# Kernel tuning notes

Hardware: AMD Instinct MI355X
Metric: run time of the kernel (lower is better)

The kernel has to match this reference:

```python
import math
import jax, jax.numpy as jnp
import numpy as np

# --- Cayley-Dickson octonion structure constants: e_i * e_j = sign * e_{i XOR j} ---
def _cd_tables(levels=3):
    idx = np.array([[0]]); sgn = np.array([[1]])
    for _ in range(levels):
        n = idx.shape[0]; N = 2 * n
        I = np.zeros((N, N), np.int64); S = np.zeros((N, N), np.int64)
        cj = lambda j: 1 if j == 0 else -1  # conj sign of basis element j
        for i in range(n):
            for j in range(n):
                I[i, j] = idx[i, j];             S[i, j] = sgn[i, j]
                I[i, n + j] = n + idx[j, i];     S[i, n + j] = sgn[j, i]
                I[n + i, j] = n + idx[i, j];     S[n + i, j] = sgn[i, j] * cj(j)
                I[n + i, n + j] = idx[j, i];     S[n + i, n + j] = -cj(j) * sgn[j, i]
        idx, sgn = I, S
    return idx, sgn

_OIDX, _OSGN = _cd_tables()
# Octonion-structured linear: out_i = sum_j SIGN[i,j] * x_j @ W[WIDX[i,j]], WIDX[i,j]=i^j
_WIDX = np.array([[i ^ j for j in range(8)] for i in range(8)], np.int64)
_SIGN = np.array([[_OSGN[j, i ^ j] for j in range(8)] for i in range(8)], np.float32)


def _oct_linear(x, W):
    # x: [B,T,C], W: [8, C/8, C/8]
    B, T, C = x.shape
    Cp = C // 8
    parts = x.reshape(B, T, 8, Cp)
    Weff = jnp.asarray(_SIGN)[:, :, None, None] * W[jnp.asarray(_WIDX)]  # [8,8,Cp,Cp]
    return jnp.einsum('btjp,ijpq->btiq', parts, Weff).reshape(B, T, C)


def _rope(x, cos, sin):
    # x: [B,T,H,D]; consecutive channel pairs form complex numbers
    B, T, H, D = x.shape
    xr = x.reshape(B, T, H, D // 2, 2)
    xe, xo = xr[..., 0], xr[..., 1]
    c = cos[None, :, None, :]
    s = sin[None, :, None, :]
    return jnp.stack([xe * c - xo * s, xe * s + xo * c], axis=-1).reshape(B, T, H, D)


def _forward(x, Wq, Wk, Wv, Wo, mixer_W, mixer_beta, freqs_cos, freqs_sin):
    B, T, C = x.shape
    H = 32; D = C // H
    q = _oct_linear(x, Wq).reshape(B, T, H, D)
    k = _oct_linear(x, Wk).reshape(B, T, H, D)
    v = _oct_linear(x, Wv).reshape(B, T, H, D)
    q = _rope(q, freqs_cos, freqs_sin)
    k = _rope(k, freqs_cos, freqs_sin)
    q = q.transpose(0, 2, 1, 3)  # [B,H,T,D]
    k = k.transpose(0, 2, 1, 3)
    v = v.transpose(0, 2, 1, 3)
    scores = jnp.einsum('bhqd,bhkd->bhqk', q, k) / jnp.sqrt(jnp.float32(D))
    mask = jnp.tril(jnp.ones((T, T), bool))
    scores = jnp.where(mask, scores, jnp.finfo(scores.dtype).min)
    y = jnp.einsum('bhqk,bhkd->bhqd', jax.nn.softmax(scores, axis=-1), v)  # [B,H,T,D]
    # octonion head mixing in groups of 8 heads
    G = H // 8
    yg = y.reshape(B, G, 8, T, D)
    Weff = jnp.asarray(_SIGN)[:, :, None, None] * mixer_W[jnp.asarray(_WIDX)]  # [8,8,D,D]
    mixed = jnp.einsum('bgjtd,ijde->bgite', yg, Weff) * mixer_beta
    y = mixed.reshape(B, H, T, D).transpose(0, 2, 1, 3).reshape(B, T, C)
    return _oct_linear(y, Wo)


def setup_inputs() -> dict:
    key = jax.random.key(0)
    ks = jax.random.split(key, 8)
    B, T, C, H = 1, 2048, 4096, 32
    D = C // H; Cp = C // 8
    x = jax.random.normal(ks[0], (B, T, C), jnp.float32)
    Wq = jax.random.normal(ks[1], (8, Cp, Cp), jnp.float32) * 0.02
    Wk = jax.random.normal(ks[2], (8, Cp, Cp), jnp.float32) * 0.02
    Wv = jax.random.normal(ks[3], (8, Cp, Cp), jnp.float32) * 0.02
    Wo = jax.random.normal(ks[4], (8, Cp, Cp), jnp.float32) * 0.02
    mixer_W = jax.random.normal(ks[5], (8, D, D), jnp.float32) * 0.02
    mixer_beta = jnp.ones((D,), jnp.float32) * np.float32(math.sqrt(3.0 / (2.0 * D)))
    half = D // 2
    inv = 1.0 / (10000.0 ** (np.arange(half) * 2.0 / D))
    ang = np.arange(T)[:, None] * inv[None, :]
    freqs_cos = jnp.asarray(np.cos(ang), jnp.float32)
    freqs_sin = jnp.asarray(np.sin(ang), jnp.float32)
    return dict(x=x, Wq=Wq, Wk=Wk, Wv=Wv, Wo=Wo, mixer_W=mixer_W,
                mixer_beta=mixer_beta, freqs_cos=freqs_cos, freqs_sin=freqs_sin)


def reference(x, Wq, Wk, Wv, Wo, mixer_W, mixer_beta, freqs_cos, freqs_sin):
    return _forward(x, Wq, Wk, Wv, Wo, mixer_W, mixer_beta, freqs_cos, freqs_sin)
```

## Files before the change

### kernel.cpp

```cpp
#include <hip/hip_runtime.h>

typedef float f32x4 __attribute__((ext_vector_type(4)));
typedef __bf16 bf16x8 __attribute__((ext_vector_type(8)));
typedef unsigned short u16;
typedef u16 u16x8 __attribute__((ext_vector_type(8)));

__constant__ float c_osgn[64] = {
  1, 1, 1, 1, 1, 1, 1, 1,
  1,-1, 1,-1, 1,-1,-1, 1,
  1,-1,-1, 1, 1, 1,-1,-1,
  1, 1,-1,-1, 1,-1, 1,-1,
  1,-1,-1,-1,-1, 1, 1, 1,
  1, 1,-1, 1,-1,-1,-1, 1,
  1, 1, 1,-1,-1, 1,-1,-1,
  1,-1, 1, 1,-1,-1, 1,-1
};

__device__ __forceinline__ u16 f2bf(float f) {
  union { float f; unsigned u; } v; v.f = f;
  unsigned u = v.u;
  return (u16)((u + 0x7fffu + ((u >> 16) & 1u)) >> 16);
}
__device__ __forceinline__ float bf2f(u16 h) {
  union { unsigned u; float f; } v; v.u = ((unsigned)h) << 16;
  return v.f;
}

typedef const __attribute__((address_space(1))) void* as1cv;
typedef __attribute__((address_space(3))) void* as3v;
__device__ __forceinline__ void load16_lds(const void* g, void* l) {
  __builtin_amdgcn_global_load_lds((as1cv)g, (as3v)l, 16, 0, 0);
}

__global__ void conv_f32_bf16_vec(const float* __restrict__ src, u16* __restrict__ dst) {
  int i = blockIdx.x * 256 + threadIdx.x;
  float4 v = ((const float4*)src)[i];
  ushort4 o; o.x = f2bf(v.x); o.y = f2bf(v.y); o.z = f2bf(v.z); o.w = f2bf(v.w);
  ((ushort4*)dst)[i] = o;
}

__global__ __launch_bounds__(256) void transpose_w2(const float* __restrict__ W,
                                                    u16* __restrict__ Wt) {
  __shared__ float t[64][65];
  const int w = blockIdx.z, p0 = blockIdx.y * 64, q0 = blockIdx.x * 64;
  const float* src = W + ((long)w * 512 + p0) * 512 + q0;
  const int tid = threadIdx.x;
  const int r = tid >> 2, c0 = (tid & 3) * 16;
#pragma unroll
  for (int j = 0; j < 4; j++) {
    float4 v = *(const float4*)(src + (long)r * 512 + c0 + j * 4);
    t[r][c0 + j * 4 + 0] = v.x; t[r][c0 + j * 4 + 1] = v.y;
    t[r][c0 + j * 4 + 2] = v.z; t[r][c0 + j * 4 + 3] = v.w;
  }
  __syncthreads();
  u16* dst = Wt + ((long)w * 512 + q0) * 512 + p0;
#pragma unroll
  for (int j = 0; j < 2; j++) {
    u16x8 o;
#pragma unroll
    for (int k = 0; k < 8; k++) o[k] = f2bf(t[c0 + j * 8 + k][r]);
    *(u16x8*)(dst + (long)r * 512 + c0 + j * 8) = o;
  }
}

__global__ void transpose_wm(const float* __restrict__ W, const float* __restrict__ beta,
                             u16* __restrict__ Wt) {
  int idx = blockIdx.x * 256 + threadIdx.x;
  int w = idx >> 14, rem = idx & 16383;
  int e = rem >> 7, d = rem & 127;
  Wt[(w << 14) + (e << 7) + d] = f2bf(W[(w << 14) + (d << 7) + e] * beta[e]);
}

template <int MODE>
__global__ __launch_bounds__(512, 2) void oct_gemm2f(
    const u16* __restrict__ A, const u16* __restrict__ WtB,
    void* __restrict__ out0, void* __restrict__ out1, void* __restrict__ out2,
    const float* __restrict__ fc, const float* __restrict__ fs,
    int K, int lda, int ldo,
    int slab_shift, int bs_shift, long wslab, long oslab, long acolslab)
{
  __shared__ u16 As[2][256][64];
  __shared__ u16 Bs[2][128][64];
  const int NT = K >> 6;
  const int BS = 1 << bs_shift;
  const long wblk = (long)BS * BS;

  const int nwg = gridDim.x * gridDim.y;
  const int lin = blockIdx.y * gridDim.x + blockIdx.x;
  const int swz = (lin & 7) * (nwg >> 3) + (lin >> 3);
  const int bx = swz % gridDim.x, by = swz / gridDim.x;

  const int nglob = bx * 128;
  const int z = nglob >> slab_shift;
  const int np = nglob & ((1 << slab_shift) - 1);
  const int bi = np >> bs_shift;
  const int nsub = np & (BS - 1);
  const int bm = by * 256;
  const u16* Wt = WtB + (long)z * wslab;
  const long acol0 = (long)z * acolslab;

  const int tid = threadIdx.x;
  const int lane = tid & 63, w = tid >> 6;
  const int l15 = lane & 15, lg = lane >> 4;
  const int wm = w >> 1, wn = w & 1;
  const int srow = lane >> 3;
  const int sgr  = (lane & 7) ^ srow;

  f32x4 acc[4][4];
#pragma unroll
  for (int a = 0; a < 4; a++)
#pragma unroll
    for (int b = 0; b < 4; b++) acc[a][b] = f32x4{0.f, 0.f, 0.f, 0.f};

  auto stage = [&](int t, int buf) {
    const int k0 = t << 6;
    const int widx = bi ^ (k0 >> bs_shift);
    const int kl = k0 & (BS - 1);
    const u16* Wsrc = Wt + (long)widx * wblk + kl;
#pragma unroll
    for (int i = 0; i < 4; i++) {
      const int r = w * 32 + i * 8;
      const u16* g = A + (long)(bm + r + srow) * lda + acol0 + k0 + sgr * 8;
      load16_lds(g, (void*)&As[buf][r][0]);
    }
#pragma unroll
    for (int i = 0; i < 2; i++) {
      const int r = w * 16 + i * 8;
      const u16* g = Wsrc + (long)(nsub + r + srow) * BS + sgr * 8;
      load16_lds(g, (void*)&Bs[buf][r][0]);
    }
  };

  stage(0, 0);
  stage(1, 1);

  for (int t = 0; t < NT; ++t) {
    if (t + 1 < NT) asm volatile("s_waitcnt vmcnt(6)" ::: "memory");
    else            asm volatile("s_waitcnt vmcnt(0)" ::: "memory");
    __builtin_amdgcn_s_barrier();
    asm volatile("" ::: "memory");

    const int cur = t & 1;
    const int bj = t >> (bs_shift - 6);
    const unsigned xm = (c_osgn[bj * 8 + (bi ^ bj)] < 0.f) ? 0x80008000u : 0u;

#pragma unroll
    for (int kk = 0; kk < 64; kk += 32) {
      const int gsw = (((kk >> 3) + lg) ^ (l15 & 7)) * 8;
      uint4 a4[4];
      bf16x8 bF[4];
#pragma unroll
      for (int mt = 0; mt < 4; mt++)
        a4[mt] = *(const uint4*)&As[cur][wm * 64 + mt * 16 + l15][gsw];
      if (xm) {
#pragma unroll
        for (int mt = 0; mt < 4; mt++) {
          a4[mt].x ^= xm; a4[mt].y ^= xm; a4[mt].z ^= xm; a4[mt].w ^= xm;
        }
      }
#pragma unroll
      for (int nt = 0; nt < 4; nt++)
        bF[nt] = *(const bf16x8*)&Bs[cur][wn * 64 + nt * 16 + l15][gsw];
#pragma unroll
      for (int mt = 0; mt < 4; mt++)
#pragma unroll
        for (int nt = 0; nt < 4; nt++)
          acc[mt][nt] = __builtin_amdgcn_mfma_f32_16x16x32_bf16(
              *(const bf16x8*)&a4[mt], bF[nt], acc[mt][nt], 0, 0, 0);
    }

    asm volatile("" ::: "memory");
    __builtin_amdgcn_s_barrier();
    asm volatile("" ::: "memory");
    if (t + 2 < NT) stage(t + 2, cur);
  }

  if constexpr (MODE == 1) {
    if (z == 2) {
      u16* vg = (u16*)out2;
#pragma unroll
      for (int mt = 0; mt < 4; mt++)
#pragma unroll
        for (int nt = 0; nt < 4; nt++)
#pragma unroll
          for (int j = 0; j < 4; j++) {
            const int row = bm + wm * 64 + mt * 16 + 4 * lg + j;
            const int col = np + wn * 64 + nt * 16 + l15;
            vg[(long)row * 4096 + col] = f2bf(acc[mt][nt][j]);
          }
    } else {
      u16* dq = (u16*)(z == 0 ? out0 : out1);
      const int h = np >> 7;
#pragma unroll
      for (int mt = 0; mt < 4; mt++)
#pragma unroll
        for (int nt = 0; nt < 4; nt++) {
          const int d = wn * 64 + nt * 16 + l15;
          const int p = d >> 1;
          const bool ev = (l15 & 1) == 0;
#pragma unroll
          for (int j = 0; j < 4; j++) {
            const int trow = bm + wm * 64 + mt * 16 + 4 * lg + j;
            const float v = acc[mt][nt][j];
            const float sh = __shfl_xor(v, 1);
            const float c = fc[trow * 64 + p];
            const float s = fs[trow * 64 + p];
            const float o = ev ? (v * c - sh * s) : (sh * s + v * c);
            dq[((long)h * 2048 + trow) * 128 + d] = f2bf(o);
          }
        }
    }
  } else {
#pragma unroll
    for (int mt = 0; mt < 4; mt++)
#pragma unroll
      for (int nt = 0; nt < 4; nt++)
#pragma unroll
        for (int j = 0; j < 4; j++) {
          const int row = bm + wm * 64 + mt * 16 + 4 * lg + j;
          const int col = np + wn * 64 + nt * 16 + l15;
          const float v = acc[mt][nt][j];
          if constexpr (MODE == 0)
            ((u16*)out0)[(long)z * oslab + (long)row * ldo + col] = f2bf(v);
          else
            ((float*)out0)[(long)row * ldo + col] = v;
        }
  }
}

__global__ void v_transpose(const u16* __restrict__ vg, u16* __restrict__ vT)
{
  int h = blockIdx.x, t0 = blockIdx.y * 64;
  __shared__ u16 lds[64][136];
  int tid = threadIdx.x;
  int rr = tid >> 4, ch = (tid & 15) * 8;
#pragma unroll
  for (int p = 0; p < 4; p++) {
    int row = p * 16 + rr;
    *(uint4*)&lds[row][ch] = *(const uint4*)(vg + (long)(t0 + row) * 4096 + h * 128 + ch);
  }
  __syncthreads();
  int dd = tid >> 3, tc = (tid & 7) * 8;
#pragma unroll
  for (int p = 0; p < 4; p++) {
    int d = p * 32 + dd;
    u16x8 o;
#pragma unroll
    for (int j = 0; j < 8; j++) o[j] = lds[tc + j][d];
    *(u16x8*)(vT + ((long)h * 128 + d) * 2048 + t0 + tc) = o;
  }
}

__global__ __launch_bounds__(256, 2) void attn3(
    const u16* __restrict__ qR, const u16* __restrict__ kR,
    const u16* __restrict__ vT, u16* __restrict__ y)
{
  const int bid = blockIdx.x;
  const int h = bid & 31;
  const int u = bid >> 5;
  const int qb = (u < 8) ? (u * 2) : (31 - u * 2);
  const int q0 = qb * 128;

  const int tid = threadIdx.x;
  const int lane = tid & 63, w = tid >> 6;
  const int l15 = lane & 15, lg = lane >> 4;

  __shared__ u16 Ks[2][64][128];
  __shared__ u16 Vs[2][128][64];
  __shared__ u16 Ps[4][32][64];

  auto stageK = [&](int kb, int buf) {
    const long kbase = (long)h * 2048 + (long)kb * 64;
#pragma unroll
    for (int i = 0; i < 4; i++) {
      const int j = w * 4 + i;
      const int row = j * 4 + (lane >> 4);
      const int sg = (lane & 15) ^ (row & 7);
      load16_lds(kR + (kbase + row) * 128 + sg * 8, (void*)&Ks[buf][j * 4][0]);
    }
  };
  auto stageV = [&](int kb, int buf) {
    const long vbase = (long)h * 128 * 2048 + (long)kb * 64;
#pragma unroll
    for (int i = 0; i < 4; i++) {
      const int j = w * 4 + i;
      const int row = j * 8 + (lane >> 3);
      const int sg = (lane & 7) ^ (row & 7);
      load16_lds(vT + vbase + (long)row * 2048 + sg * 8, (void*)&Vs[buf][j * 8][0]);
    }
  };

  stageK(0, 0);
  stageV(0, 0);

  bf16x8 aQ[2][4];
#pragma unroll
  for (int rs = 0; rs < 2; rs++) {
    const long qbase = ((long)h * 2048 + q0 + w * 32 + rs * 16 + l15) * 128;
#pragma unroll
    for (int c = 0; c < 4; c++)
      aQ[rs][c] = *(const bf16x8*)(qR + qbase + 32 * c + 8 * lg);
  }

  float m[2][4], lsum[2][4];
  f32x4 Y[2][8];
#pragma unroll
  for (int rs = 0; rs < 2; rs++)
#pragma unroll
    for (int rr = 0; rr < 4; rr++) { m[rs][rr] = -1e30f; lsum[rs][rr] = 0.f; }
#pragma unroll
  for (int rs = 0; rs < 2; rs++)
#pragma unroll
    for (int dt = 0; dt < 8; dt++) Y[rs][dt] = f32x4{0.f, 0.f, 0.f, 0.f};

  const float scale = 0.08838834764831845f;
  const int nkb = 2 * qb + 2;

  for (int kb = 0; kb < nkb; kb++) {
    const int buf = kb & 1;
    const int k0 = kb * 64;
    if (kb + 1 < nkb) { stageK(kb + 1, buf ^ 1); stageV(kb + 1, buf ^ 1); }
    if (kb + 1 < nkb) asm volatile("s_waitcnt vmcnt(8)" ::: "memory");
    else              asm volatile("s_waitcnt vmcnt(0)" ::: "memory");
    __builtin_amdgcn_s_barrier();
    asm volatile("" ::: "memory");

    f32x4 S[2][4];
#pragma unroll
    for (int rs = 0; rs < 2; rs++)
#pragma unroll
      for (int ks = 0; ks < 4; ks++) S[rs][ks] = f32x4{0.f, 0.f, 0.f, 0.f};
#pragma unroll
    for (int c = 0; c < 4; c++) {
      bf16x8 bK[4];
#pragma unroll
      for (int ks = 0; ks < 4; ks++)
        bK[ks] = *(const bf16x8*)&Ks[buf][ks * 16 + l15][(((4 * c + lg) ^ (l15 & 7)) * 8)];
#pragma unroll
      for (int rs = 0; rs < 2; rs++)
#pragma unroll
        for (int ks = 0; ks < 4; ks++)
          S[rs][ks] = __builtin_amdgcn_mfma_f32_16x16x32_bf16(aQ[rs][c], bK[ks], S[rs][ks], 0, 0, 0);
    }

#pragma unroll
    for (int rs = 0; rs < 2; rs++) {
      const int qrow0 = q0 + w * 32 + rs * 16 + 4 * lg;
#pragma unroll
      for (int ks = 0; ks < 4; ks++) {
        const int kg = k0 + ks * 16 + l15;
#pragma unroll
        for (int rr = 0; rr < 4; rr++) {
          float s = S[rs][ks][rr] * scale;
          S[rs][ks][rr] = (kg > qrow0 + rr) ? -1e30f : s;
        }
      }
      float sf[4];
      bool need = false;
#pragma unroll
      for (int rr = 0; rr < 4; rr++) {
        float mx = fmaxf(fmaxf(S[rs][0][rr], S[rs][1][rr]),
                         fmaxf(S[rs][2][rr], S[rs][3][rr]));
#pragma unroll
        for (int off = 1; off < 16; off <<= 1) mx = fmaxf(mx, __shfl_xor(mx, off));
        const bool upd = (mx > m[rs][rr] + 8.f);
        const float mn = upd ? mx : m[rs][rr];
        const float sc = upd ? __expf(m[rs][rr] - mn) : 1.f;
        need |= upd;
        m[rs][rr] = mn;
        float rsum = 0.f;
#pragma unroll
        for (int ks = 0; ks < 4; ks++) {
          float e = __expf(S[rs][ks][rr] - mn);
          S[rs][ks][rr] = e;
          rsum += e;
        }
#pragma unroll
        for (int off = 1; off < 16; off <<= 1) rsum += __shfl_xor(rsum, off);
        lsum[rs][rr] = lsum[rs][rr] * sc + rsum;
        sf[rr] = sc;
      }
      if (__any(need)) {
#pragma unroll
        for (int dt = 0; dt < 8; dt++) {
          f32x4 yv = Y[rs][dt];
          yv[0] *= sf[0]; yv[1] *= sf[1]; yv[2] *= sf[2]; yv[3] *= sf[3];
          Y[rs][dt] = yv;
        }
      }
#pragma unroll
      for (int ks = 0; ks < 4; ks++)
#pragma unroll
        for (int rr = 0; rr < 4; rr++) {
          const int row = rs * 16 + 4 * lg + rr;
          const int G = (2 * ks + (l15 >> 3)) ^ (row & 7);
          Ps[w][row][G * 8 + (l15 & 7)] = f2bf(S[rs][ks][rr]);
        }
    }

#pragma unroll
    for (int kk = 0; kk < 2; kk++) {
      const int pg = ((4 * kk + lg) ^ (l15 & 7)) * 8;
      bf16x8 pF0 = *(const bf16x8*)&Ps[w][l15][pg];
      bf16x8 pF1 = *(const bf16x8*)&Ps[w][16 + l15][pg];
#pragma unroll
      for (int dt = 0; dt < 8; dt++) {
        bf16x8 vF = *(const bf16x8*)&Vs[buf][dt * 16 + l15][pg];
        Y[0][dt] = __builtin_amdgcn_mfma_f32_16x16x32_bf16(pF0, vF, Y[0][dt], 0, 0, 0);
        Y[1][dt] = __builtin_amdgcn_mfma_f32_16x16x32_bf16(pF1, vF, Y[1][dt], 0, 0, 0);
      }
    }
    asm volatile("" ::: "memory");
    __builtin_amdgcn_s_barrier();
    asm volatile("" ::: "memory");
  }

#pragma unroll
  for (int rs = 0; rs < 2; rs++) {
    float inv[4];
#pragma unroll
    for (int rr = 0; rr < 4; rr++) inv[rr] = 1.0f / lsum[rs][rr];
#pragma unroll
    for (int dt = 0; dt < 8; dt++)
#pragma unroll
      for (int rr = 0; rr < 4; rr++)
        y[(long)(q0 + w * 32 + rs * 16 + 4 * lg + rr) * 4096 + h * 128 + dt * 16 + l15] =
            f2bf(Y[rs][dt][rr] * inv[rr]);
  }
}

extern "C" void kernel_launch(void* const* d_in, const int* in_sizes, int n_in,
                              void* d_out, int out_size, void* d_ws, size_t ws_size,
                              hipStream_t stream) {
  const float* x    = (const float*)d_in[0];
  const float* Wq   = (const float*)d_in[1];
  const float* Wk   = (const float*)d_in[2];
  const float* Wv   = (const float*)d_in[3];
  const float* Wo   = (const float*)d_in[4];
  const float* Wm   = (const float*)d_in[5];
  const float* beta = (const float*)d_in[6];
  const float* fc   = (const float*)d_in[7];
  const float* fs   = (const float*)d_in[8];
  float* out = (float*)d_out;

  const long TC = 2048L * 4096L;
  const long WSZ = 8L * 512 * 512;
  u16* ws  = (u16*)d_ws;
  u16* xb  = ws;
  u16* wt  = ws + TC;
  u16* wmt = wt + 4 * WSZ;
  u16* g3  = wmt + 131072L;
  u16* r3  = g3 + 3 * TC;
  u16* yatt = xb;
  u16* ymix = g3;

  conv_f32_bf16_vec<<<TC / 4 / 256, 256, 0, stream>>>(x, xb);
  transpose_w2<<<dim3(8, 8, 8), 256, 0, stream>>>(Wq, wt + 0 * WSZ);
  transpose_w2<<<dim3(8, 8, 8), 256, 0, stream>>>(Wk, wt + 1 * WSZ);
  transpose_w2<<<dim3(8, 8, 8), 256, 0, stream>>>(Wv, wt + 2 * WSZ);
  transpose_w2<<<dim3(8, 8, 8), 256, 0, stream>>>(Wo, wt + 3 * WSZ);
  transpose_wm<<<512, 256, 0, stream>>>(Wm, beta, wmt);

  oct_gemm2f<1><<<dim3(96, 8), 512, 0, stream>>>(
      xb, wt, (void*)r3, (void*)(r3 + TC), (void*)g3, fc, fs,
      4096, 4096, 4096, 12, 9, WSZ, 0L, 0L);

  v_transpose<<<dim3(32, 32), 256, 0, stream>>>(g3, r3 + 2 * TC);

  attn3<<<512, 256, 0, stream>>>(r3, r3 + TC, r3 + 2 * TC, yatt);

  oct_gemm2f<0><<<dim3(32, 8), 512, 0, stream>>>(
      yatt, wmt, (void*)ymix, nullptr, nullptr, nullptr, nullptr,
      1024, 4096, 4096, 10, 7, 0L, 1024L, 1024L);

  oct_gemm2f<2><<<dim3(32, 8), 512, 0, stream>>>(
      ymix, wt + 3 * WSZ, (void*)out, nullptr, nullptr, nullptr, nullptr,
      4096, 4096, 4096, 12, 9, 0L, 0L, 0L);
}
```

Measured before the change: 486.0 us.

## Switch octonion GEMMs to 128x128 tiles with single-buffered LDS, 256 threads

```diff
diff --git a/kernel.cpp b/kernel.cpp
--- a/kernel.cpp
+++ b/kernel.cpp
@@ -72,15 +72,15 @@
 }
 
 template <int MODE>
-__global__ __launch_bounds__(512, 2) void oct_gemm2f(
+__global__ __launch_bounds__(256, 3) void oct_gemm128(
     const u16* __restrict__ A, const u16* __restrict__ WtB,
     void* __restrict__ out0, void* __restrict__ out1, void* __restrict__ out2,
     const float* __restrict__ fc, const float* __restrict__ fs,
     int K, int lda, int ldo,
     int slab_shift, int bs_shift, long wslab, long oslab, long acolslab)
 {
-  __shared__ u16 As[2][256][64];
-  __shared__ u16 Bs[2][128][64];
+  __shared__ u16 As[128][64];
+  __shared__ u16 Bs[128][64];
   const int NT = K >> 6;
   const int BS = 1 << bs_shift;
   const long wblk = (long)BS * BS;
@@ -95,7 +95,7 @@
   const int np = nglob & ((1 << slab_shift) - 1);
   const int bi = np >> bs_shift;
   const int nsub = np & (BS - 1);
-  const int bm = by * 256;
+  const int bm = by * 128;
   const u16* Wt = WtB + (long)z * wslab;
   const long acol0 = (long)z * acolslab;
 
@@ -112,37 +112,26 @@
 #pragma unroll
     for (int b = 0; b < 4; b++) acc[a][b] = f32x4{0.f, 0.f, 0.f, 0.f};
 
-  auto stage = [&](int t, int buf) {
+  for (int t = 0; t < NT; ++t) {
     const int k0 = t << 6;
-    const int widx = bi ^ (k0 >> bs_shift);
-    const int kl = k0 & (BS - 1);
-    const u16* Wsrc = Wt + (long)widx * wblk + kl;
+    const int bj = k0 >> bs_shift;
+    const int widx = bi ^ bj;
+    const unsigned xm = (c_osgn[bj * 8 + widx] < 0.f) ? 0x80008000u : 0u;
+    const u16* Wsrc = Wt + (long)widx * wblk + (k0 & (BS - 1));
+
 #pragma unroll
     for (int i = 0; i < 4; i++) {
-      const int r = w * 32 + i * 8;
-      const u16* g = A + (long)(bm + r + srow) * lda + acol0 + k0 + sgr * 8;
-      load16_lds(g, (void*)&As[buf][r][0]);
-    }
-#pragma unroll
-    for (int i = 0; i < 2; i++) {
-      const int r = w * 16 + i * 8;
-      const u16* g = Wsrc + (long)(nsub + r + srow) * BS + sgr * 8;
-      load16_lds(g, (void*)&Bs[buf][r][0]);
-    }
-  };
-
-  stage(0, 0);
-  stage(1, 1);
-
-  for (int t = 0; t < NT; ++t) {
-    if (t + 1 < NT) asm volatile("s_waitcnt vmcnt(6)" ::: "memory");
-    else            asm volatile("s_waitcnt vmcnt(0)" ::: "memory");
-    __builtin_amdgcn_s_barrier();
-    asm volatile("" ::: "memory");
-
-    const int cur = t & 1;
-    const int bj = t >> (bs_shift - 6);
-    const unsigned xm = (c_osgn[bj * 8 + (bi ^ bj)] < 0.f) ? 0x80008000u : 0u;
+      const int r = (w * 4 + i) * 8;
+      load16_lds(A + (long)(bm + r + srow) * lda + acol0 + k0 + sgr * 8,
+                 (void*)&As[r][0]);
+    }
+#pragma unroll
+    for (int i = 0; i < 4; i++) {
+      const int r = (w * 4 + i) * 8;
+      load16_lds(Wsrc + (long)(nsub + r + srow) * BS + sgr * 8,
+                 (void*)&Bs[r][0]);
+    }
+    __syncthreads();
 
 #pragma unroll
     for (int kk = 0; kk < 64; kk += 32) {
@@ -151,7 +140,7 @@
       bf16x8 bF[4];
 #pragma unroll
       for (int mt = 0; mt < 4; mt++)
-        a4[mt] = *(const uint4*)&As[cur][wm * 64 + mt * 16 + l15][gsw];
+        a4[mt] = *(const uint4*)&As[wm * 64 + mt * 16 + l15][gsw];
       if (xm) {
 #pragma unroll
         for (int mt = 0; mt < 4; mt++) {
@@ -160,7 +149,7 @@
       }
 #pragma unroll
       for (int nt = 0; nt < 4; nt++)
-        bF[nt] = *(const bf16x8*)&Bs[cur][wn * 64 + nt * 16 + l15][gsw];
+        bF[nt] = *(const bf16x8*)&Bs[wn * 64 + nt * 16 + l15][gsw];
 #pragma unroll
       for (int mt = 0; mt < 4; mt++)
 #pragma unroll
@@ -168,11 +157,7 @@
           acc[mt][nt] = __builtin_amdgcn_mfma_f32_16x16x32_bf16(
               *(const bf16x8*)&a4[mt], bF[nt], acc[mt][nt], 0, 0, 0);
     }
-
-    asm volatile("" ::: "memory");
-    __builtin_amdgcn_s_barrier();
-    asm volatile("" ::: "memory");
-    if (t + 2 < NT) stage(t + 2, cur);
+    __syncthreads();
   }
 
   if constexpr (MODE == 1) {
@@ -461,7 +446,7 @@
   transpose_w2<<<dim3(8, 8, 8), 256, 0, stream>>>(Wo, wt + 3 * WSZ);
   transpose_wm<<<512, 256, 0, stream>>>(Wm, beta, wmt);
 
-  oct_gemm2f<1><<<dim3(96, 8), 512, 0, stream>>>(
+  oct_gemm128<1><<<dim3(96, 16), 256, 0, stream>>>(
       xb, wt, (void*)r3, (void*)(r3 + TC), (void*)g3, fc, fs,
       4096, 4096, 4096, 12, 9, WSZ, 0L, 0L);
 
@@ -469,11 +454,11 @@
 
   attn3<<<512, 256, 0, stream>>>(r3, r3 + TC, r3 + 2 * TC, yatt);
 
-  oct_gemm2f<0><<<dim3(32, 8), 512, 0, stream>>>(
+  oct_gemm128<0><<<dim3(32, 16), 256, 0, stream>>>(
       yatt, wmt, (void*)ymix, nullptr, nullptr, nullptr, nullptr,
       1024, 4096, 4096, 10, 7, 0L, 1024L, 1024L);
 
-  oct_gemm2f<2><<<dim3(32, 8), 512, 0, stream>>>(
+  oct_gemm128<2><<<dim3(32, 16), 256, 0, stream>>>(
       ymix, wt + 3 * WSZ, (void*)out, nullptr, nullptr, nullptr, nullptr,
       4096, 4096, 4096, 12, 9, 0L, 0L, 0L);
 }
```

After: 472.8 us. -2.7%, faster.
